# Kernel optimization log

Measured on AMD Instinct MI355X. Metric: run time of the kernel, lower is better.

Reference implementation:

```python
import jax, jax.numpy as jnp
import numpy as np

B, H, M_DIM, K, N = 4, 8, 2048, 2048, 64
NNZ = B * H * M_DIM * 64


def setup_inputs() -> dict:
    key = jax.random.key(0)
    k_val, k_b, k_bh, k_m, k_k = jax.random.split(key, 5)
    values = jax.random.normal(k_val, (NNZ,), dtype=jnp.float32)
    b = jax.random.normal(k_b, (B, H, K, N), dtype=jnp.float32)
    idx_bh = jax.random.randint(k_bh, (NNZ,), 0, B * H, dtype=jnp.int32)
    idx_m = jax.random.randint(k_m, (NNZ,), 0, M_DIM, dtype=jnp.int32)
    idx_k = jax.random.randint(k_k, (NNZ,), 0, K, dtype=jnp.int32)
    return {"values": values, "b": b, "idx_bh": idx_bh, "idx_m": idx_m,
            "idx_k": idx_k, "M": M_DIM}


def reference(values, b, idx_bh, idx_m, idx_k, M):
    # Batched sparse-dense matmul: out[b,h,m,:] = sum_k A[b,h,m,k] * b[b,h,k,:]
    # A is in COO form over flattened batch-head dim: (idx_bh, idx_m, idx_k, values).
    Bd, Hd, Kd, Nd = b.shape
    b_flat = b.reshape(Bd * Hd, Kd, Nd)             # [BH, K, N]
    # gather the dense rows each nonzero touches, scale by the sparse value
    gathered = values[:, None] * b_flat[idx_bh, idx_k]  # [nnz, N]
    # scatter-add into output rows (flat segment id = bh*M + m)
    seg = idx_bh * M + idx_m
    out = jax.ops.segment_sum(gathered, seg, num_segments=Bd * Hd * M)  # [BH*M, N]
    return out.reshape(Bd, Hd, M, Nd)
```

## Files before the change

kernel.cpp:

```cpp
#include <hip/hip_runtime.h>

constexpr int N_COLS = 64;
constexpr int K_DIM  = 2048;
constexpr int M_DIM  = 2048;
constexpr int SEGS   = 32 * 2048;
constexpr int NBUCK  = 512;
constexpr int SEG_PER_BUCK = SEGS / NBUCK;
constexpr int PART_T = 512;
constexpr int PART_E = 16;
constexpr int TILE   = PART_T * PART_E;
constexpr int CAP2   = 8192;
constexpr int CSTR   = 16;
constexpr int OVL_CAP = 640;
constexpr size_t OVFCNT_OFF = 32768;
constexpr size_t OVFBUF_OFF = 40960;
constexpr int OVF_GCAP = (int)((524288 - OVFBUF_OFF) / 8);
constexpr size_t BBF_OFF    = 524288;
constexpr size_t PACKED_OFF = BBF_OFF + 8388608;

struct Pair { float v; int k; };

__global__ void spmm_coo_atomic(const float* __restrict__ values,
                                const float* __restrict__ b,
                                const int*   __restrict__ idx_bh,
                                const int*   __restrict__ idx_m,
                                const int*   __restrict__ idx_k,
                                float*       __restrict__ out,
                                int nnz) {
    long long gid = (long long)blockIdx.x * blockDim.x + threadIdx.x;
    int nz   = (int)(gid >> 6);
    int lane = (int)(gid & 63);
    if (nz >= nnz) return;
    float bval = b[((size_t)idx_bh[nz] * K_DIM + idx_k[nz]) * N_COLS + lane];
    atomicAdd(&out[((size_t)idx_bh[nz] * M_DIM + idx_m[nz]) * N_COLS + lane],
              values[nz] * bval);
}

__global__ __launch_bounds__(256)
void conv_b(const float* __restrict__ b, unsigned int* __restrict__ bbf, int n8) {
    int i = blockIdx.x * 256 + threadIdx.x;
    if (i >= n8) return;
    const float4* s = (const float4*)b + (size_t)i * 2;
    float4 x = s[0], y = s[1];
    auto cv = [](float a, float c) {
        unsigned ua = __float_as_uint(a), uc = __float_as_uint(c);
        ua = (ua + 0x7FFFu + ((ua >> 16) & 1u)) >> 16;
        uc = (uc + 0x7FFFu + ((uc >> 16) & 1u)) >> 16;
        return ua | (uc << 16);
    };
    uint4 r = make_uint4(cv(x.x, x.y), cv(x.z, x.w), cv(y.x, y.y), cv(y.z, y.w));
    *(uint4*)(bbf + (size_t)i * 4) = r;
}

__global__ __launch_bounds__(PART_T)
void partition512(const float* __restrict__ values,
                  const int*   __restrict__ idx_bh,
                  const int*   __restrict__ idx_m,
                  const int*   __restrict__ idx_k,
                  int*  __restrict__ cursor,
                  int*  __restrict__ ovfcnt,
                  int2* __restrict__ ovf,
                  int*  __restrict__ packed, int nnz) {
    __shared__ int ebuf[TILE];
    __shared__ unsigned short bbuf[TILE];
    __shared__ int lcount[NBUCK];
    __shared__ int sc[NBUCK];
    __shared__ int lstart[NBUCK];
    __shared__ int total_s;

    int t = threadIdx.x;
    lcount[t] = 0;
    __syncthreads();

    int e0 = blockIdx.x * TILE + t * PART_E;
    int   pk[PART_E];
    short bkt[PART_E];
    short rnk[PART_E];

    auto enc = [](int vb, int k, int seg) {
        return (int)(((unsigned)(vb + 0x20000) & 0xFFFC0000u) | ((unsigned)k << 7)
                     | ((unsigned)seg & 127u));
    };

    if (e0 + PART_E <= nnz) {
        const int4* vv4 = (const int4*)(values + e0);
        const int4* bh4 = (const int4*)(idx_bh + e0);
        const int4* mm4 = (const int4*)(idx_m + e0);
        const int4* kk4 = (const int4*)(idx_k + e0);
        #pragma unroll
        for (int q = 0; q < PART_E / 4; ++q) {
            int4 vq = vv4[q];
            int4 bq = bh4[q], mq = mm4[q], kq = kk4[q];
            int s0 = bq.x * M_DIM + mq.x;
            int s1 = bq.y * M_DIM + mq.y;
            int s2 = bq.z * M_DIM + mq.z;
            int s3 = bq.w * M_DIM + mq.w;
            pk[4*q+0]=enc(vq.x,kq.x,s0); bkt[4*q+0]=(short)(s0>>7);
            rnk[4*q+0]=(short)atomicAdd(&lcount[s0>>7],1);
            pk[4*q+1]=enc(vq.y,kq.y,s1); bkt[4*q+1]=(short)(s1>>7);
            rnk[4*q+1]=(short)atomicAdd(&lcount[s1>>7],1);
            pk[4*q+2]=enc(vq.z,kq.z,s2); bkt[4*q+2]=(short)(s2>>7);
            rnk[4*q+2]=(short)atomicAdd(&lcount[s2>>7],1);
            pk[4*q+3]=enc(vq.w,kq.w,s3); bkt[4*q+3]=(short)(s3>>7);
            rnk[4*q+3]=(short)atomicAdd(&lcount[s3>>7],1);
        }
    } else {
        #pragma unroll
        for (int i = 0; i < PART_E; ++i) {
            int e = e0 + i;
            if (e < nnz) {
                int seg = idx_bh[e] * M_DIM + idx_m[e];
                int bu  = seg >> 7;
                pk[i]  = enc(__float_as_int(values[e]), idx_k[e], seg);
                bkt[i] = (short)bu;
                rnk[i] = (short)atomicAdd(&lcount[bu], 1);
            } else bkt[i] = -1;
        }
    }
    __syncthreads();

    int c = lcount[t];
    int sbase = (c > 0) ? atomicAdd(&cursor[t * CSTR], c) : 0;

    sc[t] = c;
    __syncthreads();
    for (int d = 1; d < NBUCK; d <<= 1) {
        int x = (t >= d) ? sc[t - d] : 0;
        __syncthreads();
        sc[t] += x;
        __syncthreads();
    }
    int ls = sc[t] - c;
    lstart[t] = ls;
    if (t == NBUCK - 1) total_s = sc[t];
    __syncthreads();
    sc[t] = sbase - ls;

    #pragma unroll
    for (int i = 0; i < PART_E; ++i) {
        if (bkt[i] >= 0) {
            int p = lstart[bkt[i]] + rnk[i];
            ebuf[p] = pk[i];
            bbuf[p] = (unsigned short)bkt[i];
        }
    }
    __syncthreads();

    int total = total_s;
    for (int p = t; p < total; p += PART_T) {
        int e  = ebuf[p];
        int bu = bbuf[p];
        int gpos = sc[bu] + p;
        if (gpos < CAP2) {
            packed[(size_t)bu * CAP2 + gpos] = e;
        } else {
            int o = atomicAdd(ovfcnt, 1);
            if (o < OVF_GCAP) ovf[o] = make_int2(e, bu);
        }
    }
}

__global__ __launch_bounds__(1024)
void sort_accum(const int*  __restrict__ packed,
                const int*  __restrict__ cursor,
                const int*  __restrict__ ovfcnt,
                const int2* __restrict__ ovf,
                const unsigned short* __restrict__ bbf,
                float* __restrict__ out) {
    __shared__ int ps[CAP2 + OVL_CAP + 8];
    __shared__ int ovl[OVL_CAP];
    __shared__ int h[SEG_PER_BUCK];
    __shared__ int cur[SEG_PER_BUCK];
    __shared__ int ovl_n;

    int t = threadIdx.x;
    int i   = blockIdx.x;
    int bkt = (i & 7) * 64 + (i >> 3);
    int cnt = cursor[bkt * CSTR];
    int L = cnt;
    if (L < 0)    L = 0;
    if (L > CAP2) L = CAP2;

    if (t < SEG_PER_BUCK) h[t] = 0;
    if (t == 0) ovl_n = 0;
    __syncthreads();

    const int4* src4 = (const int4*)(packed + (size_t)bkt * CAP2);
    int4 ra = src4[t * 2];
    int4 rb = src4[t * 2 + 1];
    int er[8] = { ra.x, ra.y, ra.z, ra.w, rb.x, rb.y, rb.z, rb.w };
    int base8 = t * 8;
    #pragma unroll
    for (int q = 0; q < 8; ++q)
        if (base8 + q < L) atomicAdd(&h[er[q] & 127], 1);

    int ovfN = ovfcnt[0];
    if (ovfN > OVF_GCAP) ovfN = OVF_GCAP;
    for (int o = t; o < ovfN; o += 1024) {
        int2 e = ovf[o];
        if (e.y == bkt) {
            int pos = atomicAdd(&ovl_n, 1);
            if (pos < OVL_CAP) {
                ovl[pos] = e.x;
                atomicAdd(&h[e.x & 127], 1);
            }
        }
    }
    __syncthreads();

    for (int d = 1; d < SEG_PER_BUCK; d <<= 1) {
        int x = 0;
        if (t < SEG_PER_BUCK && t >= d) x = h[t - d];
        __syncthreads();
        if (t < SEG_PER_BUCK && t >= d) h[t] += x;
        __syncthreads();
    }
    if (t < SEG_PER_BUCK) cur[t] = (t == 0) ? 0 : h[t - 1];
    __syncthreads();

    #pragma unroll
    for (int q = 0; q < 8; ++q) {
        if (base8 + q < L) {
            int pos = atomicAdd(&cur[er[q] & 127], 1);
            ps[pos] = er[q];
        }
    }
    int on = ovl_n; if (on > OVL_CAP) on = OVL_CAP;
    if (t < on) {
        int e = ovl[t];
        int pos = atomicAdd(&cur[e & 127], 1);
        ps[pos] = e;
    }
    __syncthreads();
    if (t < 8) ps[h[SEG_PER_BUCK - 1] + t] = 0;
    __syncthreads();

    int lane = t & 63;
    int w    = t >> 6;
    int bh   = bkt >> 4;
    const char* bb = (const char*)bbf + ((size_t)bh << 18);
    size_t obase = ((size_t)bkt << 13);
    int lb = lane * 2;

    for (int s = w * 8; s < w * 8 + 8; ++s) {
        int js = (s == 0) ? 0 : h[s - 1];
        int je = h[s];
        float a0 = 0.f, a1 = 0.f, a2 = 0.f, a3 = 0.f;
        int j = js;
        for (; j + 8 <= je; j += 8) {
            int s0 = __builtin_amdgcn_readfirstlane(ps[j+0]);
            int s1 = __builtin_amdgcn_readfirstlane(ps[j+1]);
            int s2 = __builtin_amdgcn_readfirstlane(ps[j+2]);
            int s3 = __builtin_amdgcn_readfirstlane(ps[j+3]);
            int s4 = __builtin_amdgcn_readfirstlane(ps[j+4]);
            int s5 = __builtin_amdgcn_readfirstlane(ps[j+5]);
            int s6 = __builtin_amdgcn_readfirstlane(ps[j+6]);
            int s7 = __builtin_amdgcn_readfirstlane(ps[j+7]);
            unsigned short u0 = *(const unsigned short*)(bb + (s0 & 0x3FF80) + lb);
            unsigned short u1 = *(const unsigned short*)(bb + (s1 & 0x3FF80) + lb);
            unsigned short u2 = *(const unsigned short*)(bb + (s2 & 0x3FF80) + lb);
            unsigned short u3 = *(const unsigned short*)(bb + (s3 & 0x3FF80) + lb);
            unsigned short u4 = *(const unsigned short*)(bb + (s4 & 0x3FF80) + lb);
            unsigned short u5 = *(const unsigned short*)(bb + (s5 & 0x3FF80) + lb);
            unsigned short u6 = *(const unsigned short*)(bb + (s6 & 0x3FF80) + lb);
            unsigned short u7 = *(const unsigned short*)(bb + (s7 & 0x3FF80) + lb);
            a0 += __int_as_float(s0 & (int)0xFFFC0000) * __int_as_float((int)u0 << 16);
            a1 += __int_as_float(s1 & (int)0xFFFC0000) * __int_as_float((int)u1 << 16);
            a2 += __int_as_float(s2 & (int)0xFFFC0000) * __int_as_float((int)u2 << 16);
            a3 += __int_as_float(s3 & (int)0xFFFC0000) * __int_as_float((int)u3 << 16);
            a0 += __int_as_float(s4 & (int)0xFFFC0000) * __int_as_float((int)u4 << 16);
            a1 += __int_as_float(s5 & (int)0xFFFC0000) * __int_as_float((int)u5 << 16);
            a2 += __int_as_float(s6 & (int)0xFFFC0000) * __int_as_float((int)u6 << 16);
            a3 += __int_as_float(s7 & (int)0xFFFC0000) * __int_as_float((int)u7 << 16);
        }
        if (j < je) {
            int s0 = __builtin_amdgcn_readfirstlane(ps[j+0]);
            int s1 = __builtin_amdgcn_readfirstlane(ps[j+1]);
            int s2 = __builtin_amdgcn_readfirstlane(ps[j+2]);
            int s3 = __builtin_amdgcn_readfirstlane(ps[j+3]);
            int s4 = __builtin_amdgcn_readfirstlane(ps[j+4]);
            int s5 = __builtin_amdgcn_readfirstlane(ps[j+5]);
            int s6 = __builtin_amdgcn_readfirstlane(ps[j+6]);
            int s7 = __builtin_amdgcn_readfirstlane(ps[j+7]);
            unsigned short u0 = *(const unsigned short*)(bb + (s0 & 0x3FF80) + lb);
            unsigned short u1 = *(const unsigned short*)(bb + (s1 & 0x3FF80) + lb);
            unsigned short u2 = *(const unsigned short*)(bb + (s2 & 0x3FF80) + lb);
            unsigned short u3 = *(const unsigned short*)(bb + (s3 & 0x3FF80) + lb);
            unsigned short u4 = *(const unsigned short*)(bb + (s4 & 0x3FF80) + lb);
            unsigned short u5 = *(const unsigned short*)(bb + (s5 & 0x3FF80) + lb);
            unsigned short u6 = *(const unsigned short*)(bb + (s6 & 0x3FF80) + lb);
            unsigned short u7 = *(const unsigned short*)(bb + (s7 & 0x3FF80) + lb);
            float v0 = (j+0 < je) ? __int_as_float(s0 & (int)0xFFFC0000) : 0.f;
            float v1 = (j+1 < je) ? __int_as_float(s1 & (int)0xFFFC0000) : 0.f;
            float v2 = (j+2 < je) ? __int_as_float(s2 & (int)0xFFFC0000) : 0.f;
            float v3 = (j+3 < je) ? __int_as_float(s3 & (int)0xFFFC0000) : 0.f;
            float v4 = (j+4 < je) ? __int_as_float(s4 & (int)0xFFFC0000) : 0.f;
            float v5 = (j+5 < je) ? __int_as_float(s5 & (int)0xFFFC0000) : 0.f;
            float v6 = (j+6 < je) ? __int_as_float(s6 & (int)0xFFFC0000) : 0.f;
            float v7 = (j+7 < je) ? __int_as_float(s7 & (int)0xFFFC0000) : 0.f;
            a0 += v0 * __int_as_float((int)u0 << 16);
            a1 += v1 * __int_as_float((int)u1 << 16);
            a2 += v2 * __int_as_float((int)u2 << 16);
            a3 += v3 * __int_as_float((int)u3 << 16);
            a0 += v4 * __int_as_float((int)u4 << 16);
            a1 += v5 * __int_as_float((int)u5 << 16);
            a2 += v6 * __int_as_float((int)u6 << 16);
            a3 += v7 * __int_as_float((int)u7 << 16);
        }
        out[obase + ((size_t)s << 6) + lane] = (a0 + a1) + (a2 + a3);
    }
}

extern "C" void kernel_launch(void* const* d_in, const int* in_sizes, int n_in,
                              void* d_out, int out_size, void* d_ws, size_t ws_size,
                              hipStream_t stream) {
    const float* values = (const float*)d_in[0];
    const float* b      = (const float*)d_in[1];
    const int*   idx_bh = (const int*)d_in[2];
    const int*   idx_m  = (const int*)d_in[3];
    const int*   idx_k  = (const int*)d_in[4];
    float*       out    = (float*)d_out;
    const int    nnz    = in_sizes[0];

    const size_t need = PACKED_OFF + (size_t)NBUCK * CAP2 * sizeof(int);

    int*  cursor = (int*)d_ws;
    int*  ovfcnt = (int*)((char*)d_ws + OVFCNT_OFF);
    int2* ovfbuf = (int2*)((char*)d_ws + OVFBUF_OFF);
    unsigned int*   bbf    = (unsigned int*)((char*)d_ws + BBF_OFF);
    int*  packed = (int*)((char*)d_ws + PACKED_OFF);

    const int nblk = (nnz + TILE - 1) / TILE;
    const int nb8  = (4 * 8 * K_DIM * N_COLS) / 8;

    if (ws_size >= need) {
        hipMemsetAsync(d_ws, 0, OVFBUF_OFF, stream);
        conv_b<<<nb8 / 256, 256, 0, stream>>>(b, bbf, nb8);
        partition512<<<nblk, PART_T, 0, stream>>>(values, idx_bh, idx_m, idx_k,
                                                  cursor, ovfcnt, ovfbuf, packed, nnz);
        sort_accum<<<NBUCK, 1024, 0, stream>>>(packed, cursor, ovfcnt, ovfbuf,
                                               (const unsigned short*)bbf, out);
    } else {
        hipMemsetAsync(d_out, 0, (size_t)out_size * sizeof(float), stream);
        long long total = (long long)nnz * N_COLS;
        spmm_coo_atomic<<<(unsigned)((total + 255) / 256), 256, 0, stream>>>(
            values, b, idx_bh, idx_m, idx_k, out, nnz);
    }
}
```

Baseline: 200.6 us.

## Replace per-bucket segment sort with fixed-point LDS atomic accumulation

The accumulate kernel no longer builds a histogram, prefix scan and counting sort of entries by output row. Each wave instead takes a contiguous chunk of staged entries and adds fixed-point integer products into a shared-memory accumulator with LDS atomics. B is pre-scaled by 2^22 before bf16 conversion, and the result is rescaled when written out as float4. The partition kernel also moves to 1024 threads with 8 elements each, guarding the bucket scan with t<NBUCK. This removes sort passes and barriers at the cost of integer truncation error, possible overflow, and LDS atomic contention.

```diff
diff --git a/kernel.cpp b/kernel.cpp
--- a/kernel.cpp
+++ b/kernel.cpp
@@ -6,8 +6,8 @@
 constexpr int SEGS   = 32 * 2048;
 constexpr int NBUCK  = 512;
 constexpr int SEG_PER_BUCK = SEGS / NBUCK;
-constexpr int PART_T = 512;
-constexpr int PART_E = 16;
+constexpr int PART_T = 1024;
+constexpr int PART_E = 8;
 constexpr int TILE   = PART_T * PART_E;
 constexpr int CAP2   = 8192;
 constexpr int CSTR   = 16;
@@ -43,7 +43,8 @@
     const float4* s = (const float4*)b + (size_t)i * 2;
     float4 x = s[0], y = s[1];
     auto cv = [](float a, float c) {
-        unsigned ua = __float_as_uint(a), uc = __float_as_uint(c);
+        unsigned ua = __float_as_uint(a * 4194304.0f);
+        unsigned uc = __float_as_uint(c * 4194304.0f);
         ua = (ua + 0x7FFFu + ((ua >> 16) & 1u)) >> 16;
         uc = (uc + 0x7FFFu + ((uc >> 16) & 1u)) >> 16;
         return ua | (uc << 16);
@@ -69,7 +70,7 @@
     __shared__ int total_s;
 
     int t = threadIdx.x;
-    lcount[t] = 0;
+    if (t < NBUCK) lcount[t] = 0;
     __syncthreads();
 
     int e0 = blockIdx.x * TILE + t * PART_E;
@@ -119,22 +120,26 @@
     }
     __syncthreads();
 
-    int c = lcount[t];
-    int sbase = (c > 0) ? atomicAdd(&cursor[t * CSTR], c) : 0;
-
-    sc[t] = c;
+    int c = (t < NBUCK) ? lcount[t] : 0;
+    int sbase = (t < NBUCK && c > 0) ? atomicAdd(&cursor[t * CSTR], c) : 0;
+
+    if (t < NBUCK) sc[t] = c;
     __syncthreads();
     for (int d = 1; d < NBUCK; d <<= 1) {
-        int x = (t >= d) ? sc[t - d] : 0;
+        int x = 0;
+        if (t < NBUCK && t >= d) x = sc[t - d];
         __syncthreads();
-        sc[t] += x;
+        if (t < NBUCK && t >= d) sc[t] += x;
         __syncthreads();
     }
-    int ls = sc[t] - c;
-    lstart[t] = ls;
-    if (t == NBUCK - 1) total_s = sc[t];
-    __syncthreads();
-    sc[t] = sbase - ls;
+    if (t < NBUCK) {
+        int ls = sc[t] - c;
+        lstart[t] = ls;
+        if (t == NBUCK - 1) total_s = sc[t];
+    }
+    __syncthreads();
+    if (t < NBUCK) sc[t] = sbase - lstart[t];
+    __syncthreads();
 
     #pragma unroll
     for (int i = 0; i < PART_E; ++i) {
@@ -167,10 +172,8 @@
                 const int2* __restrict__ ovf,
                 const unsigned short* __restrict__ bbf,
                 float* __restrict__ out) {
-    __shared__ int ps[CAP2 + OVL_CAP + 8];
-    __shared__ int ovl[OVL_CAP];
-    __shared__ int h[SEG_PER_BUCK];
-    __shared__ int cur[SEG_PER_BUCK];
+    __shared__ int stage[CAP2 + OVL_CAP + 8];
+    __shared__ int acc[SEG_PER_BUCK * N_COLS];
     __shared__ int ovl_n;
 
     int t = threadIdx.x;
@@ -181,18 +184,17 @@
     if (L < 0)    L = 0;
     if (L > CAP2) L = CAP2;
 
-    if (t < SEG_PER_BUCK) h[t] = 0;
     if (t == 0) ovl_n = 0;
-    __syncthreads();
+    int4* a4 = (int4*)acc;
+    a4[t]        = make_int4(0, 0, 0, 0);
+    a4[t + 1024] = make_int4(0, 0, 0, 0);
 
     const int4* src4 = (const int4*)(packed + (size_t)bkt * CAP2);
     int4 ra = src4[t * 2];
     int4 rb = src4[t * 2 + 1];
-    int er[8] = { ra.x, ra.y, ra.z, ra.w, rb.x, rb.y, rb.z, rb.w };
-    int base8 = t * 8;
-    #pragma unroll
-    for (int q = 0; q < 8; ++q)
-        if (base8 + q < L) atomicAdd(&h[er[q] & 127], 1);
+    *(int4*)&stage[t * 8]     = ra;
+    *(int4*)&stage[t * 8 + 4] = rb;
+    __syncthreads();
 
     int ovfN = ovfcnt[0];
     if (ovfN > OVF_GCAP) ovfN = OVF_GCAP;
@@ -200,114 +202,73 @@
         int2 e = ovf[o];
         if (e.y == bkt) {
             int pos = atomicAdd(&ovl_n, 1);
-            if (pos < OVL_CAP) {
-                ovl[pos] = e.x;
-                atomicAdd(&h[e.x & 127], 1);
-            }
-        }
-    }
-    __syncthreads();
-
-    for (int d = 1; d < SEG_PER_BUCK; d <<= 1) {
-        int x = 0;
-        if (t < SEG_PER_BUCK && t >= d) x = h[t - d];
-        __syncthreads();
-        if (t < SEG_PER_BUCK && t >= d) h[t] += x;
-        __syncthreads();
-    }
-    if (t < SEG_PER_BUCK) cur[t] = (t == 0) ? 0 : h[t - 1];
-    __syncthreads();
-
-    #pragma unroll
-    for (int q = 0; q < 8; ++q) {
-        if (base8 + q < L) {
-            int pos = atomicAdd(&cur[er[q] & 127], 1);
-            ps[pos] = er[q];
-        }
-    }
+            if (pos < OVL_CAP) stage[L + pos] = e.x;
+        }
+    }
+    __syncthreads();
     int on = ovl_n; if (on > OVL_CAP) on = OVL_CAP;
-    if (t < on) {
-        int e = ovl[t];
-        int pos = atomicAdd(&cur[e & 127], 1);
-        ps[pos] = e;
-    }
-    __syncthreads();
-    if (t < 8) ps[h[SEG_PER_BUCK - 1] + t] = 0;
+    int Lt = L + on;
+    if (t < 8) stage[Lt + t] = 0;
     __syncthreads();
 
     int lane = t & 63;
-    int w    = t >> 6;
+    int w    = __builtin_amdgcn_readfirstlane(t >> 6);
     int bh   = bkt >> 4;
     const char* bb = (const char*)bbf + ((size_t)bh << 18);
-    size_t obase = ((size_t)bkt << 13);
     int lb = lane * 2;
 
-    for (int s = w * 8; s < w * 8 + 8; ++s) {
-        int js = (s == 0) ? 0 : h[s - 1];
-        int je = h[s];
-        float a0 = 0.f, a1 = 0.f, a2 = 0.f, a3 = 0.f;
-        int j = js;
-        for (; j + 8 <= je; j += 8) {
-            int s0 = __builtin_amdgcn_readfirstlane(ps[j+0]);
-            int s1 = __builtin_amdgcn_readfirstlane(ps[j+1]);
-            int s2 = __builtin_amdgcn_readfirstlane(ps[j+2]);
-            int s3 = __builtin_amdgcn_readfirstlane(ps[j+3]);
-            int s4 = __builtin_amdgcn_readfirstlane(ps[j+4]);
-            int s5 = __builtin_amdgcn_readfirstlane(ps[j+5]);
-            int s6 = __builtin_amdgcn_readfirstlane(ps[j+6]);
-            int s7 = __builtin_amdgcn_readfirstlane(ps[j+7]);
-            unsigned short u0 = *(const unsigned short*)(bb + (s0 & 0x3FF80) + lb);
-            unsigned short u1 = *(const unsigned short*)(bb + (s1 & 0x3FF80) + lb);
-            unsigned short u2 = *(const unsigned short*)(bb + (s2 & 0x3FF80) + lb);
-            unsigned short u3 = *(const unsigned short*)(bb + (s3 & 0x3FF80) + lb);
-            unsigned short u4 = *(const unsigned short*)(bb + (s4 & 0x3FF80) + lb);
-            unsigned short u5 = *(const unsigned short*)(bb + (s5 & 0x3FF80) + lb);
-            unsigned short u6 = *(const unsigned short*)(bb + (s6 & 0x3FF80) + lb);
-            unsigned short u7 = *(const unsigned short*)(bb + (s7 & 0x3FF80) + lb);
-            a0 += __int_as_float(s0 & (int)0xFFFC0000) * __int_as_float((int)u0 << 16);
-            a1 += __int_as_float(s1 & (int)0xFFFC0000) * __int_as_float((int)u1 << 16);
-            a2 += __int_as_float(s2 & (int)0xFFFC0000) * __int_as_float((int)u2 << 16);
-            a3 += __int_as_float(s3 & (int)0xFFFC0000) * __int_as_float((int)u3 << 16);
-            a0 += __int_as_float(s4 & (int)0xFFFC0000) * __int_as_float((int)u4 << 16);
-            a1 += __int_as_float(s5 & (int)0xFFFC0000) * __int_as_float((int)u5 << 16);
-            a2 += __int_as_float(s6 & (int)0xFFFC0000) * __int_as_float((int)u6 << 16);
-            a3 += __int_as_float(s7 & (int)0xFFFC0000) * __int_as_float((int)u7 << 16);
-        }
-        if (j < je) {
-            int s0 = __builtin_amdgcn_readfirstlane(ps[j+0]);
-            int s1 = __builtin_amdgcn_readfirstlane(ps[j+1]);
-            int s2 = __builtin_amdgcn_readfirstlane(ps[j+2]);
-            int s3 = __builtin_amdgcn_readfirstlane(ps[j+3]);
-            int s4 = __builtin_amdgcn_readfirstlane(ps[j+4]);
-            int s5 = __builtin_amdgcn_readfirstlane(ps[j+5]);
-            int s6 = __builtin_amdgcn_readfirstlane(ps[j+6]);
-            int s7 = __builtin_amdgcn_readfirstlane(ps[j+7]);
-            unsigned short u0 = *(const unsigned short*)(bb + (s0 & 0x3FF80) + lb);
-            unsigned short u1 = *(const unsigned short*)(bb + (s1 & 0x3FF80) + lb);
-            unsigned short u2 = *(const unsigned short*)(bb + (s2 & 0x3FF80) + lb);
-            unsigned short u3 = *(const unsigned short*)(bb + (s3 & 0x3FF80) + lb);
-            unsigned short u4 = *(const unsigned short*)(bb + (s4 & 0x3FF80) + lb);
-            unsigned short u5 = *(const unsigned short*)(bb + (s5 & 0x3FF80) + lb);
-            unsigned short u6 = *(const unsigned short*)(bb + (s6 & 0x3FF80) + lb);
-            unsigned short u7 = *(const unsigned short*)(bb + (s7 & 0x3FF80) + lb);
-            float v0 = (j+0 < je) ? __int_as_float(s0 & (int)0xFFFC0000) : 0.f;
-            float v1 = (j+1 < je) ? __int_as_float(s1 & (int)0xFFFC0000) : 0.f;
-            float v2 = (j+2 < je) ? __int_as_float(s2 & (int)0xFFFC0000) : 0.f;
-            float v3 = (j+3 < je) ? __int_as_float(s3 & (int)0xFFFC0000) : 0.f;
-            float v4 = (j+4 < je) ? __int_as_float(s4 & (int)0xFFFC0000) : 0.f;
-            float v5 = (j+5 < je) ? __int_as_float(s5 & (int)0xFFFC0000) : 0.f;
-            float v6 = (j+6 < je) ? __int_as_float(s6 & (int)0xFFFC0000) : 0.f;
-            float v7 = (j+7 < je) ? __int_as_float(s7 & (int)0xFFFC0000) : 0.f;
-            a0 += v0 * __int_as_float((int)u0 << 16);
-            a1 += v1 * __int_as_float((int)u1 << 16);
-            a2 += v2 * __int_as_float((int)u2 << 16);
-            a3 += v3 * __int_as_float((int)u3 << 16);
-            a0 += v4 * __int_as_float((int)u4 << 16);
-            a1 += v5 * __int_as_float((int)u5 << 16);
-            a2 += v6 * __int_as_float((int)u6 << 16);
-            a3 += v7 * __int_as_float((int)u7 << 16);
-        }
-        out[obase + ((size_t)s << 6) + lane] = (a0 + a1) + (a2 + a3);
+    int G  = (Lt + 127) >> 7;
+    int ws = w * (G << 3);
+    int we = ws + (G << 3);
+    if (we > Lt) we = Lt;
+
+    const int4* st4 = (const int4*)stage;
+    for (int j = ws; j < we; j += 8) {
+        int4 g0 = st4[(j >> 2) + 0];
+        int4 g1 = st4[(j >> 2) + 1];
+        int s0 = __builtin_amdgcn_readfirstlane(g0.x);
+        int s1 = __builtin_amdgcn_readfirstlane(g0.y);
+        int s2 = __builtin_amdgcn_readfirstlane(g0.z);
+        int s3 = __builtin_amdgcn_readfirstlane(g0.w);
+        int s4 = __builtin_amdgcn_readfirstlane(g1.x);
+        int s5 = __builtin_amdgcn_readfirstlane(g1.y);
+        int s6 = __builtin_amdgcn_readfirstlane(g1.z);
+        int s7 = __builtin_amdgcn_readfirstlane(g1.w);
+        unsigned short u0 = *(const unsigned short*)(bb + (s0 & 0x3FF80) + lb);
+        unsigned short u1 = *(const unsigned short*)(bb + (s1 & 0x3FF80) + lb);
+        unsigned short u2 = *(const unsigned short*)(bb + (s2 & 0x3FF80) + lb);
+        unsigned short u3 = *(const unsigned short*)(bb + (s3 & 0x3FF80) + lb);
+        unsigned short u4 = *(const unsigned short*)(bb + (s4 & 0x3FF80) + lb);
+        unsigned short u5 = *(const unsigned short*)(bb + (s5 & 0x3FF80) + lb);
+        unsigned short u6 = *(const unsigned short*)(bb + (s6 & 0x3FF80) + lb);
+        unsigned short u7 = *(const unsigned short*)(bb + (s7 & 0x3FF80) + lb);
+        int p0 = (int)(__int_as_float(s0 & (int)0xFFFC0000) * __int_as_float((int)u0 << 16));
+        int p1 = (int)(__int_as_float(s1 & (int)0xFFFC0000) * __int_as_float((int)u1 << 16));
+        int p2 = (int)(__int_as_float(s2 & (int)0xFFFC0000) * __int_as_float((int)u2 << 16));
+        int p3 = (int)(__int_as_float(s3 & (int)0xFFFC0000) * __int_as_float((int)u3 << 16));
+        int p4 = (int)(__int_as_float(s4 & (int)0xFFFC0000) * __int_as_float((int)u4 << 16));
+        int p5 = (int)(__int_as_float(s5 & (int)0xFFFC0000) * __int_as_float((int)u5 << 16));
+        int p6 = (int)(__int_as_float(s6 & (int)0xFFFC0000) * __int_as_float((int)u6 << 16));
+        int p7 = (int)(__int_as_float(s7 & (int)0xFFFC0000) * __int_as_float((int)u7 << 16));
+        atomicAdd(&acc[((s0 & 127) << 6) + lane], p0);
+        atomicAdd(&acc[((s1 & 127) << 6) + lane], p1);
+        atomicAdd(&acc[((s2 & 127) << 6) + lane], p2);
+        atomicAdd(&acc[((s3 & 127) << 6) + lane], p3);
+        atomicAdd(&acc[((s4 & 127) << 6) + lane], p4);
+        atomicAdd(&acc[((s5 & 127) << 6) + lane], p5);
+        atomicAdd(&acc[((s6 & 127) << 6) + lane], p6);
+        atomicAdd(&acc[((s7 & 127) << 6) + lane], p7);
+    }
+    __syncthreads();
+
+    float4* o4 = (float4*)(out + ((size_t)bkt << 13));
+    const float ks = 1.0f / 4194304.0f;
+    #pragma unroll
+    for (int q = 0; q < 2; ++q) {
+        int idx = t + q * 1024;
+        int4 av = a4[idx];
+        o4[idx] = make_float4((float)av.x * ks, (float)av.y * ks,
+                              (float)av.z * ks, (float)av.w * ks);
     }
 }
 
@@ -327,7 +288,7 @@
     int*  cursor = (int*)d_ws;
     int*  ovfcnt = (int*)((char*)d_ws + OVFCNT_OFF);
     int2* ovfbuf = (int2*)((char*)d_ws + OVFBUF_OFF);
-    unsigned int*   bbf    = (unsigned int*)((char*)d_ws + BBF_OFF);
+    unsigned int* bbf = (unsigned int*)((char*)d_ws + BBF_OFF);
     int*  packed = (int*)((char*)d_ws + PACKED_OFF);
 
     const int nblk = (nnz + TILE - 1) / TILE;
```

Result: no change. 203.1 us (+1.2%).

## Replace global-atomic bucket scatter with per-block tile offsets and fused bf16 conversion

Applied to the files above, without the earlier changes.

The partition kernel no longer scatters entries into global bucket arrays with atomic cursors and an overflow buffer. Each block now writes its locally bucket-sorted tile contiguously and records per-bucket offsets, and the accumulation kernel gathers its bucket's slices from every tile through a prefix sum over those offsets. The separate B-to-bf16 conversion kernel and the workspace memset are folded into the partition kernel, which removes two launches. In exchange, the gather reads many short scattered slices, and the per-bucket capacity (CAP) is a fixed bound with entries beyond it dropped silently.

```diff
diff --git a/kernel.cpp b/kernel.cpp
--- a/kernel.cpp
+++ b/kernel.cpp
@@ -6,19 +6,12 @@
 constexpr int SEGS   = 32 * 2048;
 constexpr int NBUCK  = 512;
 constexpr int SEG_PER_BUCK = SEGS / NBUCK;
-constexpr int PART_T = 512;
-constexpr int PART_E = 16;
+constexpr int PART_T = 1024;
+constexpr int PART_E = 8;
 constexpr int TILE   = PART_T * PART_E;
-constexpr int CAP2   = 8192;
-constexpr int CSTR   = 16;
-constexpr int OVL_CAP = 640;
-constexpr size_t OVFCNT_OFF = 32768;
-constexpr size_t OVFBUF_OFF = 40960;
-constexpr int OVF_GCAP = (int)((524288 - OVFBUF_OFF) / 8);
-constexpr size_t BBF_OFF    = 524288;
-constexpr size_t PACKED_OFF = BBF_OFF + 8388608;
-
-struct Pair { float v; int k; };
+constexpr int CAP    = 8960;
+constexpr int OSTR   = 520;
+
 
 __global__ void spmm_coo_atomic(const float* __restrict__ values,
                                 const float* __restrict__ b,
@@ -36,43 +29,43 @@
               values[nz] * bval);
 }
 
-__global__ __launch_bounds__(256)
-void conv_b(const float* __restrict__ b, unsigned int* __restrict__ bbf, int n8) {
-    int i = blockIdx.x * 256 + threadIdx.x;
-    if (i >= n8) return;
-    const float4* s = (const float4*)b + (size_t)i * 2;
-    float4 x = s[0], y = s[1];
-    auto cv = [](float a, float c) {
-        unsigned ua = __float_as_uint(a), uc = __float_as_uint(c);
-        ua = (ua + 0x7FFFu + ((ua >> 16) & 1u)) >> 16;
-        uc = (uc + 0x7FFFu + ((uc >> 16) & 1u)) >> 16;
-        return ua | (uc << 16);
-    };
-    uint4 r = make_uint4(cv(x.x, x.y), cv(x.z, x.w), cv(y.x, y.y), cv(y.z, y.w));
-    *(uint4*)(bbf + (size_t)i * 4) = r;
-}
-
 __global__ __launch_bounds__(PART_T)
 void partition512(const float* __restrict__ values,
                   const int*   __restrict__ idx_bh,
                   const int*   __restrict__ idx_m,
                   const int*   __restrict__ idx_k,
-                  int*  __restrict__ cursor,
-                  int*  __restrict__ ovfcnt,
-                  int2* __restrict__ ovf,
-                  int*  __restrict__ packed, int nnz) {
+                  const float* __restrict__ b,
+                  unsigned int* __restrict__ bbf,
+                  int*  __restrict__ offt,
+                  int*  __restrict__ tiles,
+                  int nnz, int nblk) {
     __shared__ int ebuf[TILE];
-    __shared__ unsigned short bbuf[TILE];
     __shared__ int lcount[NBUCK];
     __shared__ int sc[NBUCK];
     __shared__ int lstart[NBUCK];
     __shared__ int total_s;
 
-    int t = threadIdx.x;
-    lcount[t] = 0;
-    __syncthreads();
-
-    int e0 = blockIdx.x * TILE + t * PART_E;
+    int t   = threadIdx.x;
+    int bid = blockIdx.x;
+
+    for (int sl = bid; sl < 512; sl += nblk) {
+        size_t base = (size_t)sl * 8192 + (size_t)t * 8;
+        const float4* s = (const float4*)(b + base);
+        float4 x = s[0], y = s[1];
+        auto cv = [](float a, float c) {
+            unsigned ua = __float_as_uint(a), uc = __float_as_uint(c);
+            ua = (ua + 0x7FFFu + ((ua >> 16) & 1u)) >> 16;
+            uc = (uc + 0x7FFFu + ((uc >> 16) & 1u)) >> 16;
+            return ua | (uc << 16);
+        };
+        uint4 r = make_uint4(cv(x.x, x.y), cv(x.z, x.w), cv(y.x, y.y), cv(y.z, y.w));
+        *(uint4*)(bbf + base / 2) = r;
+    }
+
+    if (t < NBUCK) lcount[t] = 0;
+    __syncthreads();
+
+    int e0 = bid * TILE + t * PART_E;
     int   pk[PART_E];
     short bkt[PART_E];
     short rnk[PART_E];
@@ -119,94 +112,102 @@
     }
     __syncthreads();
 
-    int c = lcount[t];
-    int sbase = (c > 0) ? atomicAdd(&cursor[t * CSTR], c) : 0;
-
-    sc[t] = c;
+    int c = (t < NBUCK) ? lcount[t] : 0;
+
+    if (t < NBUCK) sc[t] = c;
     __syncthreads();
     for (int d = 1; d < NBUCK; d <<= 1) {
-        int x = (t >= d) ? sc[t - d] : 0;
-        __syncthreads();
-        sc[t] += x;
-        __syncthreads();
-    }
-    int ls = sc[t] - c;
-    lstart[t] = ls;
-    if (t == NBUCK - 1) total_s = sc[t];
-    __syncthreads();
-    sc[t] = sbase - ls;
+        int x = 0;
+        if (t < NBUCK && t >= d) x = sc[t - d];
+        __syncthreads();
+        if (t < NBUCK && t >= d) sc[t] += x;
+        __syncthreads();
+    }
+    if (t < NBUCK) {
+        int ls = sc[t] - c;
+        lstart[t] = ls;
+        if (t == NBUCK - 1) total_s = sc[t];
+    }
+    __syncthreads();
+
+    if (t < NBUCK) offt[(size_t)bid * OSTR + t] = lstart[t];
+    if (t == NBUCK) offt[(size_t)bid * OSTR + NBUCK] = total_s;
 
     #pragma unroll
     for (int i = 0; i < PART_E; ++i) {
-        if (bkt[i] >= 0) {
-            int p = lstart[bkt[i]] + rnk[i];
-            ebuf[p] = pk[i];
-            bbuf[p] = (unsigned short)bkt[i];
-        }
-    }
-    __syncthreads();
-
-    int total = total_s;
-    for (int p = t; p < total; p += PART_T) {
-        int e  = ebuf[p];
-        int bu = bbuf[p];
-        int gpos = sc[bu] + p;
-        if (gpos < CAP2) {
-            packed[(size_t)bu * CAP2 + gpos] = e;
-        } else {
-            int o = atomicAdd(ovfcnt, 1);
-            if (o < OVF_GCAP) ovf[o] = make_int2(e, bu);
-        }
-    }
+        if (bkt[i] >= 0)
+            ebuf[lstart[bkt[i]] + rnk[i]] = pk[i];
+    }
+    __syncthreads();
+
+    int4* tp = (int4*)(tiles + (size_t)bid * TILE);
+    const int4* eb4 = (const int4*)ebuf;
+    tp[t]        = eb4[t];
+    tp[t + 1024] = eb4[t + 1024];
 }
 
 __global__ __launch_bounds__(1024)
-void sort_accum(const int*  __restrict__ packed,
-                const int*  __restrict__ cursor,
-                const int*  __restrict__ ovfcnt,
-                const int2* __restrict__ ovf,
+void sort_accum(const int* __restrict__ tiles,
+                const int* __restrict__ offt,
                 const unsigned short* __restrict__ bbf,
-                float* __restrict__ out) {
-    __shared__ int ps[CAP2 + OVL_CAP + 8];
-    __shared__ int ovl[OVL_CAP];
+                float* __restrict__ out, int nblk) {
+    __shared__ int stage[CAP];
+    __shared__ int ps[CAP + 8];
     __shared__ int h[SEG_PER_BUCK];
     __shared__ int cur[SEG_PER_BUCK];
-    __shared__ int ovl_n;
+    __shared__ int sc[NBUCK];
+    __shared__ int pf[NBUCK + 1];
+    __shared__ int ro[NBUCK];
 
     int t = threadIdx.x;
     int i   = blockIdx.x;
     int bkt = (i & 7) * 64 + (i >> 3);
-    int cnt = cursor[bkt * CSTR];
-    int L = cnt;
-    if (L < 0)    L = 0;
-    if (L > CAP2) L = CAP2;
 
     if (t < SEG_PER_BUCK) h[t] = 0;
-    if (t == 0) ovl_n = 0;
-    __syncthreads();
-
-    const int4* src4 = (const int4*)(packed + (size_t)bkt * CAP2);
-    int4 ra = src4[t * 2];
-    int4 rb = src4[t * 2 + 1];
-    int er[8] = { ra.x, ra.y, ra.z, ra.w, rb.x, rb.y, rb.z, rb.w };
-    int base8 = t * 8;
-    #pragma unroll
-    for (int q = 0; q < 8; ++q)
-        if (base8 + q < L) atomicAdd(&h[er[q] & 127], 1);
-
-    int ovfN = ovfcnt[0];
-    if (ovfN > OVF_GCAP) ovfN = OVF_GCAP;
-    for (int o = t; o < ovfN; o += 1024) {
-        int2 e = ovf[o];
-        if (e.y == bkt) {
-            int pos = atomicAdd(&ovl_n, 1);
-            if (pos < OVL_CAP) {
-                ovl[pos] = e.x;
-                atomicAdd(&h[e.x & 127], 1);
+
+    int cA = 0, cB = 0;
+    if (t < NBUCK) {
+        if (t < nblk) {
+            cA = offt[(size_t)t * OSTR + bkt];
+            cB = offt[(size_t)t * OSTR + bkt + 1];
+        }
+        ro[t] = cA;
+        sc[t] = cB - cA;
+    }
+    __syncthreads();
+    for (int d = 1; d < NBUCK; d <<= 1) {
+        int x = 0;
+        if (t < NBUCK && t >= d) x = sc[t - d];
+        __syncthreads();
+        if (t < NBUCK && t >= d) sc[t] += x;
+        __syncthreads();
+    }
+    if (t < NBUCK) {
+        pf[t + 1] = sc[t];
+        if (t == 0) pf[0] = 0;
+    }
+    __syncthreads();
+
+    int lane = t & 63;
+    int w    = t >> 6;
+    for (int r = 0; r < 32; ++r) {
+        int bsrc = w * 32 + r;
+        int s0  = pf[bsrc];
+        int len = pf[bsrc + 1] - s0;
+        const int* src = tiles + (size_t)bsrc * TILE + ro[bsrc];
+        for (int e = lane; e < len; e += 64) {
+            int val = src[e];
+            int dst = s0 + e;
+            if (dst < CAP) {
+                stage[dst] = val;
+                atomicAdd(&h[val & 127], 1);
             }
         }
     }
     __syncthreads();
+
+    int Lt = pf[NBUCK];
+    if (Lt > CAP) Lt = CAP;
 
     for (int d = 1; d < SEG_PER_BUCK; d <<= 1) {
         int x = 0;
@@ -218,26 +219,16 @@
     if (t < SEG_PER_BUCK) cur[t] = (t == 0) ? 0 : h[t - 1];
     __syncthreads();
 
-    #pragma unroll
-    for (int q = 0; q < 8; ++q) {
-        if (base8 + q < L) {
-            int pos = atomicAdd(&cur[er[q] & 127], 1);
-            ps[pos] = er[q];
-        }
-    }
-    int on = ovl_n; if (on > OVL_CAP) on = OVL_CAP;
-    if (t < on) {
-        int e = ovl[t];
+    for (int idx = t; idx < Lt; idx += 1024) {
+        int e = stage[idx];
         int pos = atomicAdd(&cur[e & 127], 1);
         ps[pos] = e;
     }
     __syncthreads();
-    if (t < 8) ps[h[SEG_PER_BUCK - 1] + t] = 0;
-    __syncthreads();
-
-    int lane = t & 63;
-    int w    = t >> 6;
-    int bh   = bkt >> 4;
+    if (t < 8) ps[Lt + t] = 0;
+    __syncthreads();
+
+    int bh = bkt >> 4;
     const char* bb = (const char*)bbf + ((size_t)bh << 18);
     size_t obase = ((size_t)bkt << 13);
     int lb = lane * 2;
@@ -322,24 +313,22 @@
     float*       out    = (float*)d_out;
     const int    nnz    = in_sizes[0];
 
-    const size_t need = PACKED_OFF + (size_t)NBUCK * CAP2 * sizeof(int);
-
-    int*  cursor = (int*)d_ws;
-    int*  ovfcnt = (int*)((char*)d_ws + OVFCNT_OFF);
-    int2* ovfbuf = (int2*)((char*)d_ws + OVFBUF_OFF);
-    unsigned int*   bbf    = (unsigned int*)((char*)d_ws + BBF_OFF);
-    int*  packed = (int*)((char*)d_ws + PACKED_OFF);
-
     const int nblk = (nnz + TILE - 1) / TILE;
-    const int nb8  = (4 * 8 * K_DIM * N_COLS) / 8;
-
-    if (ws_size >= need) {
-        hipMemsetAsync(d_ws, 0, OVFBUF_OFF, stream);
-        conv_b<<<nb8 / 256, 256, 0, stream>>>(b, bbf, nb8);
+
+    const size_t offt_sz   = (size_t)nblk * OSTR * sizeof(int);
+    const size_t bbf_off   = (offt_sz + 255) & ~(size_t)255;
+    const size_t tiles_off = bbf_off + 8388608;
+    const size_t need      = tiles_off + (size_t)nblk * TILE * sizeof(int);
+
+    int* offt = (int*)d_ws;
+    unsigned int* bbf = (unsigned int*)((char*)d_ws + bbf_off);
+    int* tiles = (int*)((char*)d_ws + tiles_off);
+
+    if (ws_size >= need && nblk <= NBUCK) {
         partition512<<<nblk, PART_T, 0, stream>>>(values, idx_bh, idx_m, idx_k,
-                                                  cursor, ovfcnt, ovfbuf, packed, nnz);
-        sort_accum<<<NBUCK, 1024, 0, stream>>>(packed, cursor, ovfcnt, ovfbuf,
-                                               (const unsigned short*)bbf, out);
+                                                  b, bbf, offt, tiles, nnz, nblk);
+        sort_accum<<<NBUCK, 1024, 0, stream>>>(tiles, offt,
+                                               (const unsigned short*)bbf, out, nblk);
     } else {
         hipMemsetAsync(d_out, 0, (size_t)out_size * sizeof(float), stream);
         long long total = (long long)nnz * N_COLS;
```

Measured after the change: 184.4 us. 1.09x faster.
